# Kernel tuning notes

Hardware: AMD Instinct MI355X
Metric: run time of the kernel (lower is better)

Reference implementation:

```python
import jax, jax.numpy as jnp
import numpy as np

N = 100000      # nodes
E = 1600000     # edges (before self-loops)
D_IN = 128      # node_attr_size
H = 4           # gat_heads
C = 32          # hidden_size (per-head out channels)
F = H * C       # feature_size = 128
K = 16          # num_clusters
L = 2           # num_gat_layers
EPS = 1e-5
NEG_SLOPE = 0.2  # PyG GATv2Conv default leaky_relu slope


def setup_inputs() -> dict:
    key = jax.random.key(0)
    ks = jax.random.split(key, 8)
    x = jax.random.normal(ks[0], (N, D_IN), jnp.float32)
    edge_index = jax.random.randint(ks[1], (2, E), 0, N, jnp.int32)
    sF = 1.0 / np.sqrt(F).astype(np.float32)
    Wp = jax.random.normal(ks[2], (D_IN, F), jnp.float32) * (1.0 / np.sqrt(D_IN).astype(np.float32))
    bp = jnp.zeros((F,), jnp.float32)
    ln_g = jnp.ones((L, F), jnp.float32)
    ln_b = jnp.zeros((L, F), jnp.float32)
    Wl = jax.random.normal(ks[3], (L, F, H * C), jnp.float32) * sF
    bl = jnp.zeros((L, H * C), jnp.float32)
    Wr = jax.random.normal(ks[4], (L, F, H * C), jnp.float32) * sF
    br = jnp.zeros((L, H * C), jnp.float32)
    att = jax.random.normal(ks[5], (L, H, C), jnp.float32) * (1.0 / np.sqrt(C).astype(np.float32))
    gb = jnp.zeros((L, F), jnp.float32)  # GATv2Conv output bias
    Wc = jax.random.normal(ks[6], (F, K), jnp.float32) * sF
    bc = jnp.zeros((K,), jnp.float32)
    return dict(x=x, edge_index=edge_index, Wp=Wp, bp=bp, ln_g=ln_g, ln_b=ln_b,
                Wl=Wl, bl=bl, Wr=Wr, br=br, att=att, gb=gb, Wc=Wc, bc=bc)


def _layernorm(x, g, b):
    mu = jnp.mean(x, axis=-1, keepdims=True)
    var = jnp.var(x, axis=-1, keepdims=True)
    return (x - mu) * jax.lax.rsqrt(var + EPS) * g + b


def reference(x, edge_index, Wp, bp, ln_g, ln_b, Wl, bl, Wr, br, att, gb, Wc, bc):
    # GATv2Conv adds self-loops by default
    loops = jnp.arange(N, dtype=edge_index.dtype)
    src = jnp.concatenate([edge_index[0], loops])  # message source j
    dst = jnp.concatenate([edge_index[1], loops])  # message target i

    h = x @ Wp + bp  # node_feat_proj -> [N, F]
    for i in range(L):
        identity = h
        hn = _layernorm(h, ln_g[i], ln_b[i])
        x_l = (hn @ Wl[i] + bl[i]).reshape(N, H, C)  # source transform
        x_r = (hn @ Wr[i] + br[i]).reshape(N, H, C)  # target transform
        m = x_l[src] + x_r[dst]                       # [E+N, H, C]
        s = jnp.where(m > 0, m, NEG_SLOPE * m)        # leaky_relu(0.2)
        logits = jnp.einsum('ehc,hc->eh', s, att[i])  # [E+N, H]
        # segment softmax over incoming edges of each target node
        mx = jax.ops.segment_max(logits, dst, num_segments=N)
        a = jnp.exp(logits - mx[dst])
        den = jax.ops.segment_sum(a, dst, num_segments=N)
        alpha = a / den[dst]
        out = jax.ops.segment_sum(x_l[src] * alpha[:, :, None], dst, num_segments=N)
        out = out.reshape(N, F) + gb[i]
        # relu activation, dropout identity (eval), residual add
        h = jax.nn.relu(out) + identity

    classification_output = h @ Wc + bc
    return (classification_output, h)
```

## Files before the change

kernel.cpp:

```cpp
#include <hip/hip_runtime.h>
#include <hip/hip_bf16.h>
#include <math.h>
#include <stdint.h>

#define N_NODES 100000
#define N_EDGES 1600000
#define ET (N_EDGES + N_NODES)
#define FDIM 128
#define NK 16
#define EPS 1e-5f
#define SLOPE 0.2f

typedef __attribute__((ext_vector_type(8))) short bf16x8;
typedef __attribute__((ext_vector_type(4))) float f32x4;
typedef __attribute__((ext_vector_type(2))) _Float16 h2;

__device__ inline unsigned pk_bf16(float a, float b) {
    float2 f; f.x = a; f.y = b;
    __hip_bfloat162 t = __float22bfloat162_rn(f);
    return *reinterpret_cast<unsigned*>(&t);
}
__device__ inline h2 as_h2(unsigned u) { return __builtin_bit_cast(h2, u); }
__device__ inline unsigned as_u(h2 v) { return __builtin_bit_cast(unsigned, v); }

#define DPPF(X, CTRL) __int_as_float(__builtin_amdgcn_mov_dpp(__float_as_int(X), (CTRL), 0xF, 0xF, true))
#define DX1(X) DPPF(X, 0xB1)
#define DX2(X) DPPF(X, 0x4E)
#define DR4(X) DPPF(X, 0x124)
#define DR8(X) DPPF(X, 0x128)
#define DB0(X) DPPF(X, 0x00)
#define DB1(X) DPPF(X, 0x55)
#define DB2(X) DPPF(X, 0xAA)
#define DB3(X) DPPF(X, 0xFF)

__device__ inline float exp2_hw(float x) {
    float r;
    asm("v_exp_f32 %0, %1" : "=v"(r) : "v"(x));
    return r;
}

#define FMAMIX_LO(ACC, U, W) \
    asm("v_fma_mix_f32 %0, %1, %2, %0 op_sel_hi:[1,0,0]" : "+v"(ACC) : "v"(U), "v"(W))
#define FMAMIX_HI(ACC, U, W) \
    asm("v_fma_mix_f32 %0, %1, %2, %0 op_sel:[1,0,0] op_sel_hi:[1,0,0]" : "+v"(ACC) : "v"(U), "v"(W))

__device__ inline int rflm(int v) { return __builtin_amdgcn_readfirstlane(v) & 131071; }


#define NBKT 196
#define BSH 9
#define BSTRIDE 10240
#define P1_EPT 8
#define P1_EPB (256 * P1_EPT)

__global__ __launch_bounds__(256) void part_kernel(const int* __restrict__ ei,
                                                   int* __restrict__ gcount,
                                                   int* __restrict__ staging) {
    __shared__ int hist[NBKT];
    __shared__ int lofs[NBKT];
    __shared__ int gbase[NBKT];
    __shared__ int s[256];
    __shared__ int spk[P1_EPB];
    __shared__ short sbk[P1_EPB];
    int t = threadIdx.x;
    if (t < NBKT) hist[t] = 0;
    __syncthreads();
    int e0 = blockIdx.x * P1_EPB + t;
    int pk[P1_EPT], bk[P1_EPT], rk[P1_EPT];
#pragma unroll
    for (int k = 0; k < P1_EPT; k++) {
        int e = e0 + k * 256;
        bk[k] = -1;
        if (e < ET) {
            int src, dst;
            if (e < N_EDGES) { src = ei[e]; dst = ei[N_EDGES + e]; }
            else             { src = dst = e - N_EDGES; }
            int b = dst >> BSH;
            pk[k] = (src << BSH) | (dst & 511);
            bk[k] = b;
            rk[k] = atomicAdd(&hist[b], 1);
        }
    }
    __syncthreads();
    int v = (t < NBKT) ? hist[t] : 0;
    s[t] = v;
    __syncthreads();
    for (int o = 1; o < 256; o <<= 1) {
        int add = (t >= o) ? s[t - o] : 0;
        __syncthreads();
        s[t] += add;
        __syncthreads();
    }
    if (t < NBKT) {
        lofs[t] = s[t] - v;
        gbase[t] = (v > 0) ? atomicAdd(&gcount[t], v) : 0;
    }
    __syncthreads();
#pragma unroll
    for (int k = 0; k < P1_EPT; k++) {
        if (bk[k] >= 0) {
            int idx = lofs[bk[k]] + rk[k];
            spk[idx] = pk[k];
            sbk[idx] = (short)bk[k];
        }
    }
    __syncthreads();
    int tot = lofs[NBKT - 1] + hist[NBKT - 1];
    for (int i = t; i < tot; i += 256) {
        int b = sbk[i];
        staging[b * BSTRIDE + gbase[b] + (i - lofs[b])] = spk[i];
    }
}

__global__ __launch_bounds__(1024) void bucket_csr_kernel(
        const int* __restrict__ staging, const int* __restrict__ gcount,
        int* __restrict__ off, int* __restrict__ perm) {
    __shared__ int hist[512];
    __shared__ int scn[512];
    __shared__ int cur[512];
    __shared__ int gpre[256];
    int b = blockIdx.x;
    int t = threadIdx.x;
    if (t < 512) hist[t] = 0;
    if (t < 256) gpre[t] = (t < NBKT) ? gcount[t] : 0;
    __syncthreads();
    int sz = gcount[b];
    for (int k = t; k < sz; k += 1024)
        atomicAdd(&hist[staging[b * BSTRIDE + k] & 511], 1);
    __syncthreads();
    int v = (t < 512) ? hist[t] : 0;
    if (t < 512) scn[t] = v;
    __syncthreads();
    for (int o = 1; o < 512; o <<= 1) {
        int add = 0, gadd = 0;
        int tg = t - 512;
        if (t < 512 && t >= o) add = scn[t - o];
        if (tg >= o && tg < 256 && o < 256) gadd = gpre[tg - o];
        __syncthreads();
        if (t < 512) scn[t] += add;
        if (tg >= o && tg < 256 && o < 256) gpre[tg] += gadd;
        __syncthreads();
    }
    int base = gpre[b] - sz;
    if (t < 512) {
        int excl = scn[t] - v;
        int n = (b << BSH) + t;
        if (n < N_NODES) off[n] = base + excl;
        cur[t] = excl;
    }
    if (b == 0 && t == 0) off[N_NODES] = ET;
    __syncthreads();
    for (int k = t; k < sz; k += 1024) {
        int p = staging[b * BSTRIDE + k];
        int slot = atomicAdd(&cur[p & 511], 1);
        perm[base + slot] = p >> BSH;
    }
}


__global__ void swizzle_kernel(const float* __restrict__ Wp,
                               const float* __restrict__ Wl,
                               const float* __restrict__ Wr,
                               ushort* __restrict__ wbp,
                               ushort* __restrict__ wbl0,
                               ushort* __restrict__ wbl1) {
    int bb = blockIdx.x, t = threadIdx.x;
    const float *W0, *W1; ushort* out; int nt;
    if (bb < 8)       { W0 = Wp; W1 = Wp; out = wbp; nt = bb; }
    else if (bb < 24) { W0 = Wl; W1 = Wr; out = wbl0; nt = bb - 8; }
    else              { W0 = Wl + FDIM * FDIM; W1 = Wr + FDIM * FDIM; out = wbl1; nt = bb - 24; }
    int kk = t >> 6, lane = t & 63;
    int n = nt * 16 + (lane & 15);
    int k0 = kk * 32 + (lane >> 4) * 8;
    const float* W = (n < 128) ? (W0 + n) : (W1 + (n - 128));
    float f[8];
#pragma unroll
    for (int j = 0; j < 8; j++) f[j] = W[(size_t)(k0 + j) * FDIM];
    uint4 u;
    u.x = pk_bf16(f[0], f[1]); u.y = pk_bf16(f[2], f[3]);
    u.z = pk_bf16(f[4], f[5]); u.w = pk_bf16(f[6], f[7]);
    *(uint4*)&out[(size_t)((nt * 4 + kk) * 64 + lane) * 8] = u;
}


__global__ __launch_bounds__(256) void ln_gemm2_kernel(
        const float* __restrict__ h,
        const float* __restrict__ g, const float* __restrict__ b,
        const ushort* __restrict__ wb, const float* __restrict__ bl,
        const float* __restrict__ br,
        ushort* __restrict__ xlh, ushort* __restrict__ xrh) {
    __shared__ uint4 fragbuf[4 * 272];
    int wid = (blockIdx.x * 256 + threadIdx.x) >> 6;
    int lane = threadIdx.x & 63;
    if (wid >= N_NODES / 16) return;
    uint4* fb = fragbuf + (threadIdx.x >> 6) * 272;
    int q = lane >> 4, m = lane & 15;
    int row0 = wid * 16;
    const float* hrow = h + (size_t)(row0 + m) * FDIM + q * 32;
    float v[32];
#pragma unroll
    for (int i = 0; i < 8; i++) {
        float4 t4 = *(const float4*)&hrow[i * 4];
        v[i * 4 + 0] = t4.x; v[i * 4 + 1] = t4.y; v[i * 4 + 2] = t4.z; v[i * 4 + 3] = t4.w;
    }
    float s = 0.f, ss = 0.f;
#pragma unroll
    for (int i = 0; i < 32; i++) { s += v[i]; ss += v[i] * v[i]; }
    s  += __shfl_xor(s, 16);  s  += __shfl_xor(s, 32);
    ss += __shfl_xor(ss, 16); ss += __shfl_xor(ss, 32);
    float mu = s * (1.f / 128.f);
    float var = ss * (1.f / 128.f) - mu * mu;
    float rv = rsqrtf(var + EPS);
#pragma unroll
    for (int i = 0; i < 8; i++) {
        float4 gv = *(const float4*)&g[q * 32 + i * 4];
        float4 bv = *(const float4*)&b[q * 32 + i * 4];
        v[i * 4 + 0] = (v[i * 4 + 0] - mu) * rv * gv.x + bv.x;
        v[i * 4 + 1] = (v[i * 4 + 1] - mu) * rv * gv.y + bv.y;
        v[i * 4 + 2] = (v[i * 4 + 2] - mu) * rv * gv.z + bv.z;
        v[i * 4 + 3] = (v[i * 4 + 3] - mu) * rv * gv.w + bv.w;
    }
#pragma unroll
    for (int p = 0; p < 4; p++) {
        uint4 u;
        u.x = pk_bf16(v[p * 8 + 0], v[p * 8 + 1]);
        u.y = pk_bf16(v[p * 8 + 2], v[p * 8 + 3]);
        u.z = pk_bf16(v[p * 8 + 4], v[p * 8 + 5]);
        u.w = pk_bf16(v[p * 8 + 6], v[p * 8 + 7]);
        fb[q * 68 + p * 17 + m] = u;
    }
    bf16x8 A[4];
#pragma unroll
    for (int kk = 0; kk < 4; kk++)
        A[kk] = *(const bf16x8*)&fb[kk * 68 + q * 17 + m];
    const bf16x8* wbv = (const bf16x8*)wb;
    f32x4 acc[16];
    f32x4 z = {0.f, 0.f, 0.f, 0.f};
#pragma unroll
    for (int nt = 0; nt < 16; nt++) acc[nt] = z;
#pragma unroll
    for (int nt = 0; nt < 16; nt++) {
#pragma unroll
        for (int kk = 0; kk < 4; kk++) {
            bf16x8 B = wbv[(nt * 4 + kk) * 64 + lane];
            acc[nt] = __builtin_amdgcn_mfma_f32_16x16x32_bf16(A[kk], B, acc[nt], 0, 0, 0);
        }
    }
#pragma unroll
    for (int nt = 0; nt < 16; nt++) {
        int col = nt * 16 + m;
        if (nt < 8) {
            float bias = bl[col];
#pragma unroll
            for (int r = 0; r < 4; r++) {
                _Float16 hf = (_Float16)(acc[nt][r] + bias);
                xlh[(size_t)(row0 + q * 4 + r) * FDIM + col] = __builtin_bit_cast(ushort, hf);
            }
        } else {
            int c2 = col - 128;
            float bias = br[c2];
#pragma unroll
            for (int r = 0; r < 4; r++) {
                _Float16 hf = (_Float16)(acc[nt][r] + bias);
                xrh[(size_t)(row0 + q * 4 + r) * FDIM + c2] = __builtin_bit_cast(ushort, hf);
            }
        }
    }
}

__global__ __launch_bounds__(256) void proj_kernel(
        const float* __restrict__ x, const ushort* __restrict__ wb,
        const float* __restrict__ bp, float* __restrict__ h) {
    __shared__ uint4 fragbuf[4 * 272];
    int wid = (blockIdx.x * 256 + threadIdx.x) >> 6;
    int lane = threadIdx.x & 63;
    if (wid >= N_NODES / 16) return;
    uint4* fb = fragbuf + (threadIdx.x >> 6) * 272;
    int q = lane >> 4, m = lane & 15;
    int row0 = wid * 16;
    const float* xrow = x + (size_t)(row0 + m) * FDIM + q * 32;
#pragma unroll
    for (int p = 0; p < 4; p++) {
        float4 a = *(const float4*)&xrow[p * 8];
        float4 c = *(const float4*)&xrow[p * 8 + 4];
        uint4 u;
        u.x = pk_bf16(a.x, a.y); u.y = pk_bf16(a.z, a.w);
        u.z = pk_bf16(c.x, c.y); u.w = pk_bf16(c.z, c.w);
        fb[q * 68 + p * 17 + m] = u;
    }
    bf16x8 A[4];
#pragma unroll
    for (int kk = 0; kk < 4; kk++)
        A[kk] = *(const bf16x8*)&fb[kk * 68 + q * 17 + m];
    const bf16x8* wbv = (const bf16x8*)wb;
    f32x4 acc[8];
    f32x4 z = {0.f, 0.f, 0.f, 0.f};
#pragma unroll
    for (int nt = 0; nt < 8; nt++) acc[nt] = z;
#pragma unroll
    for (int nt = 0; nt < 8; nt++) {
#pragma unroll
        for (int kk = 0; kk < 4; kk++) {
            bf16x8 B = wbv[(nt * 4 + kk) * 64 + lane];
            acc[nt] = __builtin_amdgcn_mfma_f32_16x16x32_bf16(A[kk], B, acc[nt], 0, 0, 0);
        }
    }
#pragma unroll
    for (int nt = 0; nt < 8; nt++) {
        int col = nt * 16 + m;
        float bias = bp[col];
#pragma unroll
        for (int r = 0; r < 4; r++)
            h[(size_t)(row0 + q * 4 + r) * FDIM + col] = acc[nt][r] + bias;
    }
}

__global__ __launch_bounds__(256) void final_kernel(const float* __restrict__ h,
                                                    const float* __restrict__ Wc,
                                                    const float* __restrict__ bc,
                                                    float* __restrict__ out) {
    __shared__ float sh[16][128];
    int row0 = blockIdx.x * 16;
    int t = threadIdx.x;
    for (int i = t; i < 512; i += 256) {
        int r = i >> 5, c4 = (i & 31) * 4;
        *(float4*)&sh[r][c4] = *(const float4*)&h[(size_t)(row0 + r) * FDIM + c4];
    }
    __syncthreads();
    int m = t >> 4, k = t & 15;
    float acc = 0.f;
    for (int c = 0; c < 128; c += 4) {
        const float4 xv = *(const float4*)&sh[m][c];
        acc += xv.x * Wc[(c + 0) * NK + k] + xv.y * Wc[(c + 1) * NK + k]
             + xv.z * Wc[(c + 2) * NK + k] + xv.w * Wc[(c + 3) * NK + k];
    }
    out[(size_t)(row0 + m) * NK + k] = acc + bc[k];
}


__global__ __launch_bounds__(256) void gat_agg_kernel(
        const unsigned* __restrict__ xlp, const unsigned* __restrict__ xrp,
        const int* __restrict__ off, const int* __restrict__ perm,
        const float* __restrict__ att, const float* __restrict__ gb,
        float* __restrict__ h) {
    int wave = (blockIdx.x * 256 + threadIdx.x) >> 6;
    unsigned lane = threadIdx.x & 63;
    int iA = wave * 2;
    if (iA >= N_NODES) return;
    int iB = iA + 1;
    int2 oA = *(const int2*)&off[iA];
    int eB2 = off[iB + 1];
    h2 xrvA = as_h2(xrp[(unsigned)iA * 64u + lane]);
    h2 xrvB = as_h2(xrp[(unsigned)iB * 64u + lane]);
    const float2 hidA = *(const float2*)&h[(size_t)iA * FDIM + lane * 2];
    const float2 hidB = *(const float2*)&h[(size_t)iB * FDIM + lane * 2];
    const float2 gbv = *(const float2*)&gb[lane * 2];
    float2 attf = *(const float2*)&att[lane * 2];
    h2 attp; attp[0] = (_Float16)(attf.x * 1.44269504f);
    attp[1] = (_Float16)(attf.y * 1.44269504f);
    const h2 c06 = {(_Float16)0.6f, (_Float16)0.6f};
    const h2 c04 = {(_Float16)0.4f, (_Float16)0.4f};
    bool b0 = lane & 1, b1 = lane & 2;
    int begA = __builtin_amdgcn_readfirstlane(oA.x);
    int endA = __builtin_amdgcn_readfirstlane(oA.y);
    int begB = endA;
    int endB = __builtin_amdgcn_readfirstlane(eB2);
    const char* xlB_ = (const char*)xlp;
    unsigned laneB = lane << 2;

#define GLD(J) (*(const unsigned*)(xlB_ + ((unsigned)(J) * 256u + laneB)))

#define EDGE_PARTIAL(XRV, U, T)                                     \
    {                                                               \
        h2 mm = as_h2(U) + XRV;                                     \
        h2 am = as_h2(as_u(mm) & 0x7FFF7FFFu);                      \
        h2 sv = am * c04 + mm * c06;                                \
        T = __builtin_amdgcn_fdot2(sv, attp, 0.f, false);           \
    }

#define COMPUTE4(S, U0, U1, U2, U3)                                 \
    {                                                               \
        float t0, t1, t2, t3;                                       \
        EDGE_PARTIAL(xrv##S, U0, t0);                               \
        EDGE_PARTIAL(xrv##S, U1, t1);                               \
        EDGE_PARTIAL(xrv##S, U2, t2);                               \
        EDGE_PARTIAL(xrv##S, U3, t3);                               \
        float u   = b0 ? t1 : t0;                                   \
        float uu2 = b0 ? t0 : t1;                                   \
        u += DX1(uu2);                                              \
        float vv  = b0 ? t3 : t2;                                   \
        float vv2 = b0 ? t2 : t3;                                   \
        vv += DX1(vv2);                                             \
        float ww  = b1 ? vv : u;                                    \
        float ww2 = b1 ? u : vv;                                    \
        ww += DX2(ww2);                                             \
        ww += DR4(ww);                                              \
        ww += DR8(ww);                                              \
        float ew = exp2_hw(ww);                                     \
        dloc##S += ew;                                              \
        float w0 = DB0(ew);                                         \
        float w1 = DB1(ew);                                         \
        float w2 = DB2(ew);                                         \
        float w3 = DB3(ew);                                         \
        FMAMIX_LO(accx##S, U0, w0); FMAMIX_HI(accy##S, U0, w0);     \
        FMAMIX_LO(accx##S, U1, w1); FMAMIX_HI(accy##S, U1, w1);     \
        FMAMIX_LO(accx##S, U2, w2); FMAMIX_HI(accy##S, U2, w2);     \
        FMAMIX_LO(accx##S, U3, w3); FMAMIX_HI(accy##S, U3, w3);     \
    }

#define TAIL1(S, U)                                                 \
    {                                                               \
        float tt;                                                   \
        EDGE_PARTIAL(xrv##S, U, tt);                                \
        tt += DX1(tt);                                              \
        tt += DX2(tt);                                              \
        tt += DR4(tt);                                              \
        tt += DR8(tt);                                              \
        float w = exp2_hw(tt);                                      \
        if ((lane & 3) == 0) dloc##S += w;                          \
        FMAMIX_LO(accx##S, U, w); FMAMIX_HI(accy##S, U, w);         \
    }

    int nbA = (endA - begA) >> 2, tlA = (endA - begA) & 3;
    int nbB = (endB - begB) >> 2, tlB = (endB - begB) & 3;
    float accxA = 0.f, accyA = 0.f, dlocA = 0.f;
    float accxB = 0.f, accyB = 0.f, dlocB = 0.f;
    unsigned c0A, c1A, c2A, c3A, d0A, d1A, d2A, d3A; int4 p2A;
    unsigned c0B, c1B, c2B, c3B, d0B, d1B, d2B, d3B; int4 p2B;
    unsigned t0A = 0, t1A = 0, t2A = 0, t0B = 0, t1B = 0, t2B = 0;
    int4 p0A, p1A, ptA, p0B, p1B, ptB;

    if (nbA > 0) {
        __builtin_memcpy(&p0A, perm + begA, 16);
        __builtin_memcpy(&p1A, perm + begA + 4, 16);
        __builtin_memcpy(&p2A, perm + begA + 8, 16);
    }
    if (tlA > 0) __builtin_memcpy(&ptA, perm + begA + 4 * nbA, 16);
    if (nbB > 0) {
        __builtin_memcpy(&p0B, perm + begB, 16);
        __builtin_memcpy(&p1B, perm + begB + 4, 16);
        __builtin_memcpy(&p2B, perm + begB + 8, 16);
    }
    if (tlB > 0) __builtin_memcpy(&ptB, perm + begB + 4 * nbB, 16);
    if (nbA > 0) {
        c0A = GLD(rflm(p0A.x)); c1A = GLD(rflm(p0A.y)); c2A = GLD(rflm(p0A.z)); c3A = GLD(rflm(p0A.w));
        d0A = GLD(rflm(p1A.x)); d1A = GLD(rflm(p1A.y)); d2A = GLD(rflm(p1A.z)); d3A = GLD(rflm(p1A.w));
    }
    if (nbB > 0) {
        c0B = GLD(rflm(p0B.x)); c1B = GLD(rflm(p0B.y)); c2B = GLD(rflm(p0B.z)); c3B = GLD(rflm(p0B.w));
        d0B = GLD(rflm(p1B.x)); d1B = GLD(rflm(p1B.y)); d2B = GLD(rflm(p1B.z)); d3B = GLD(rflm(p1B.w));
    }
    if (tlA > 0) {
        t0A = GLD(rflm(ptA.x));
        if (tlA > 1) t1A = GLD(rflm(ptA.y));
        if (tlA > 2) t2A = GLD(rflm(ptA.z));
    }
    if (tlB > 0) {
        t0B = GLD(rflm(ptB.x));
        if (tlB > 1) t1B = GLD(rflm(ptB.y));
        if (tlB > 2) t2B = GLD(rflm(ptB.z));
    }

    int blkA = 0, blkB = 0;
    while (blkA + 2 < nbA && blkB + 2 < nbB) {
        unsigned e0 = GLD(rflm(p2A.x)), e1 = GLD(rflm(p2A.y));
        unsigned e2 = GLD(rflm(p2A.z)), e3 = GLD(rflm(p2A.w));
        unsigned f0 = GLD(rflm(p2B.x)), f1 = GLD(rflm(p2B.y));
        unsigned f2 = GLD(rflm(p2B.z)), f3 = GLD(rflm(p2B.w));
        __builtin_memcpy(&p2A, perm + begA + 4 * blkA + 12, 16);
        __builtin_memcpy(&p2B, perm + begB + 4 * blkB + 12, 16);
        COMPUTE4(A, c0A, c1A, c2A, c3A);
        c0A = d0A; c1A = d1A; c2A = d2A; c3A = d3A;
        d0A = e0; d1A = e1; d2A = e2; d3A = e3;
        COMPUTE4(B, c0B, c1B, c2B, c3B);
        c0B = d0B; c1B = d1B; c2B = d2B; c3B = d3B;
        d0B = f0; d1B = f1; d2B = f2; d3B = f3;
        ++blkA; ++blkB;
    }
    for (; blkA + 2 < nbA; ++blkA) {
        unsigned e0 = GLD(rflm(p2A.x)), e1 = GLD(rflm(p2A.y));
        unsigned e2 = GLD(rflm(p2A.z)), e3 = GLD(rflm(p2A.w));
        __builtin_memcpy(&p2A, perm + begA + 4 * blkA + 12, 16);
        COMPUTE4(A, c0A, c1A, c2A, c3A);
        c0A = d0A; c1A = d1A; c2A = d2A; c3A = d3A;
        d0A = e0; d1A = e1; d2A = e2; d3A = e3;
    }
    for (; blkB + 2 < nbB; ++blkB) {
        unsigned f0 = GLD(rflm(p2B.x)), f1 = GLD(rflm(p2B.y));
        unsigned f2 = GLD(rflm(p2B.z)), f3 = GLD(rflm(p2B.w));
        __builtin_memcpy(&p2B, perm + begB + 4 * blkB + 12, 16);
        COMPUTE4(B, c0B, c1B, c2B, c3B);
        c0B = d0B; c1B = d1B; c2B = d2B; c3B = d3B;
        d0B = f0; d1B = f1; d2B = f2; d3B = f3;
    }
    if (nbA >= 2) {
        COMPUTE4(A, c0A, c1A, c2A, c3A);
        c0A = d0A; c1A = d1A; c2A = d2A; c3A = d3A;
    }
    if (nbB >= 2) {
        COMPUTE4(B, c0B, c1B, c2B, c3B);
        c0B = d0B; c1B = d1B; c2B = d2B; c3B = d3B;
    }
    if (nbA >= 1) COMPUTE4(A, c0A, c1A, c2A, c3A);
    if (nbB >= 1) COMPUTE4(B, c0B, c1B, c2B, c3B);
    if (tlA > 0) {
        TAIL1(A, t0A);
        if (tlA > 1) TAIL1(A, t1A);
        if (tlA > 2) TAIL1(A, t2A);
    }
    if (tlB > 0) {
        TAIL1(B, t0B);
        if (tlB > 1) TAIL1(B, t1B);
        if (tlB > 2) TAIL1(B, t2B);
    }
#undef EDGE_PARTIAL
#undef COMPUTE4
#undef TAIL1
#undef GLD

    float denA = dlocA + DX1(dlocA);
    denA += DX2(denA);
    float invA = 1.f / denA;
    float2 resA;
    resA.x = fmaxf(accxA * invA + gbv.x, 0.f) + hidA.x;
    resA.y = fmaxf(accyA * invA + gbv.y, 0.f) + hidA.y;
    *(float2*)&h[(size_t)iA * FDIM + lane * 2] = resA;
    float denB = dlocB + DX1(dlocB);
    denB += DX2(denB);
    float invB = 1.f / denB;
    float2 resB;
    resB.x = fmaxf(accxB * invB + gbv.x, 0.f) + hidB.x;
    resB.y = fmaxf(accyB * invB + gbv.y, 0.f) + hidB.y;
    *(float2*)&h[(size_t)iB * FDIM + lane * 2] = resB;
}


extern "C" void kernel_launch(void* const* d_in, const int* in_sizes, int n_in,
                              void* d_out, int out_size, void* d_ws, size_t ws_size,
                              hipStream_t stream) {
    const float* x    = (const float*)d_in[0];
    const int*   ei   = (const int*)  d_in[1];
    const float* Wp   = (const float*)d_in[2];
    const float* bp   = (const float*)d_in[3];
    const float* ln_g = (const float*)d_in[4];
    const float* ln_b = (const float*)d_in[5];
    const float* Wl   = (const float*)d_in[6];
    const float* bl   = (const float*)d_in[7];
    const float* Wr   = (const float*)d_in[8];
    const float* br   = (const float*)d_in[9];
    const float* att  = (const float*)d_in[10];
    const float* gb   = (const float*)d_in[11];
    const float* Wc   = (const float*)d_in[12];
    const float* bc   = (const float*)d_in[13];

    float* out_cls = (float*)d_out;
    float* h = out_cls + (size_t)N_NODES * NK;

    char* w = (char*)d_ws;
    int* off    = (int*)w; w += (size_t)(N_NODES + 1) * sizeof(int);
    int* gcount = (int*)w; w += 256 * sizeof(int);
    int* perm   = (int*)w; w += (size_t)ET * sizeof(int);
    uintptr_t a = ((uintptr_t)w + 255) & ~(uintptr_t)255;
    ushort* xlh = (ushort*)a;
    ushort* xrh = xlh + (size_t)N_NODES * FDIM;
    ushort* wbp = xrh + (size_t)N_NODES * FDIM;
    ushort* wbl0 = wbp + 8 * 4 * 64 * 8;
    ushort* wbl1 = wbl0 + 16 * 4 * 64 * 8;
    int* staging = (int*)xlh;

    swizzle_kernel<<<40, 256, 0, stream>>>(Wp, Wl, Wr, wbp, wbl0, wbl1);

    hipMemsetAsync(gcount, 0, NBKT * sizeof(int), stream);
    part_kernel<<<(ET + P1_EPB - 1) / P1_EPB, 256, 0, stream>>>(ei, gcount, staging);
    bucket_csr_kernel<<<NBKT, 1024, 0, stream>>>(staging, gcount, off, perm);

    const int gw = (N_NODES / 16 + 3) / 4;
    proj_kernel<<<gw, 256, 0, stream>>>(x, wbp, bp, h);

    for (int l = 0; l < 2; ++l) {
        ln_gemm2_kernel<<<gw, 256, 0, stream>>>(
            h, ln_g + l * FDIM, ln_b + l * FDIM,
            (l == 0) ? wbl0 : wbl1, bl + l * FDIM, br + l * FDIM,
            xlh, xrh);
        gat_agg_kernel<<<(N_NODES / 2) / 4, 256, 0, stream>>>(
            (const unsigned*)xlh, (const unsigned*)xrh, off, perm,
            att + l * FDIM, gb + l * FDIM, h);
    }

    final_kernel<<<N_NODES / 16, 256, 0, stream>>>(h, Wc, bc, out_cls);
}
```

Before: 451.8 us.

## Merge setup kernels: fuse weight swizzle into partition, projection into CSR build

Folds the weight-swizzle kernel into the edge-partition kernel as extra blocks, and runs the input projection GEMM as extra blocks of the bucket CSR kernel, which drops from 1024 to 256 threads and scans two histogram entries per thread. This cuts two kernel launches and lets independent work overlap within one grid. In exchange the CSR blocks have fewer threads for their histogram and scatter loops, and the block types compete for shared memory and occupancy.

```diff
diff --git a/kernel.cpp b/kernel.cpp
--- a/kernel.cpp
+++ b/kernel.cpp
@@ -52,20 +52,44 @@
 #define BSTRIDE 10240
 #define P1_EPT 8
 #define P1_EPB (256 * P1_EPT)
-
-__global__ __launch_bounds__(256) void part_kernel(const int* __restrict__ ei,
-                                                   int* __restrict__ gcount,
-                                                   int* __restrict__ staging) {
+#define PART_BLOCKS ((ET + P1_EPB - 1) / P1_EPB)
+
+__global__ __launch_bounds__(256) void prep_kernel(
+        const int* __restrict__ ei, int* __restrict__ gcount,
+        int* __restrict__ staging,
+        const float* __restrict__ Wp, const float* __restrict__ Wl,
+        const float* __restrict__ Wr, ushort* __restrict__ wbp,
+        ushort* __restrict__ wbl0, ushort* __restrict__ wbl1) {
     __shared__ int hist[NBKT];
     __shared__ int lofs[NBKT];
     __shared__ int gbase[NBKT];
     __shared__ int s[256];
     __shared__ int spk[P1_EPB];
     __shared__ short sbk[P1_EPB];
+    int bid = blockIdx.x;
     int t = threadIdx.x;
+    if (bid >= PART_BLOCKS) {
+        int bb = bid - PART_BLOCKS;
+        const float *W0, *W1; ushort* out; int nt;
+        if (bb < 8)       { W0 = Wp; W1 = Wp; out = wbp; nt = bb; }
+        else if (bb < 24) { W0 = Wl; W1 = Wr; out = wbl0; nt = bb - 8; }
+        else              { W0 = Wl + FDIM * FDIM; W1 = Wr + FDIM * FDIM; out = wbl1; nt = bb - 24; }
+        int kk = t >> 6, lane = t & 63;
+        int n = nt * 16 + (lane & 15);
+        int k0 = kk * 32 + (lane >> 4) * 8;
+        const float* W = (n < 128) ? (W0 + n) : (W1 + (n - 128));
+        float f[8];
+#pragma unroll
+        for (int j = 0; j < 8; j++) f[j] = W[(size_t)(k0 + j) * FDIM];
+        uint4 u;
+        u.x = pk_bf16(f[0], f[1]); u.y = pk_bf16(f[2], f[3]);
+        u.z = pk_bf16(f[4], f[5]); u.w = pk_bf16(f[6], f[7]);
+        *(uint4*)&out[(size_t)((nt * 4 + kk) * 64 + lane) * 8] = u;
+        return;
+    }
     if (t < NBKT) hist[t] = 0;
     __syncthreads();
-    int e0 = blockIdx.x * P1_EPB + t;
+    int e0 = bid * P1_EPB + t;
     int pk[P1_EPT], bk[P1_EPT], rk[P1_EPT];
 #pragma unroll
     for (int k = 0; k < P1_EPT; k++) {
@@ -112,74 +136,95 @@
     }
 }
 
-__global__ __launch_bounds__(1024) void bucket_csr_kernel(
+__global__ __launch_bounds__(256) void csr_proj_kernel(
         const int* __restrict__ staging, const int* __restrict__ gcount,
-        int* __restrict__ off, int* __restrict__ perm) {
-    __shared__ int hist[512];
-    __shared__ int scn[512];
-    __shared__ int cur[512];
-    __shared__ int gpre[256];
-    int b = blockIdx.x;
+        int* __restrict__ off, int* __restrict__ perm,
+        const float* __restrict__ x, const ushort* __restrict__ wb,
+        const float* __restrict__ bp, float* __restrict__ h) {
+    __shared__ uint4 fragbuf[4 * 272];
+    int bid = blockIdx.x;
     int t = threadIdx.x;
-    if (t < 512) hist[t] = 0;
-    if (t < 256) gpre[t] = (t < NBKT) ? gcount[t] : 0;
+    if (bid >= NBKT) {
+        int wid = ((bid - NBKT) * 256 + t) >> 6;
+        int lane = t & 63;
+        if (wid >= N_NODES / 16) return;
+        uint4* fb = fragbuf + (t >> 6) * 272;
+        int q = lane >> 4, m = lane & 15;
+        int row0 = wid * 16;
+        const float* xrow = x + (size_t)(row0 + m) * FDIM + q * 32;
+#pragma unroll
+        for (int p = 0; p < 4; p++) {
+            float4 a = *(const float4*)&xrow[p * 8];
+            float4 c = *(const float4*)&xrow[p * 8 + 4];
+            uint4 u;
+            u.x = pk_bf16(a.x, a.y); u.y = pk_bf16(a.z, a.w);
+            u.z = pk_bf16(c.x, c.y); u.w = pk_bf16(c.z, c.w);
+            fb[q * 68 + p * 17 + m] = u;
+        }
+        bf16x8 A[4];
+#pragma unroll
+        for (int kk = 0; kk < 4; kk++)
+            A[kk] = *(const bf16x8*)&fb[kk * 68 + q * 17 + m];
+        const bf16x8* wbv = (const bf16x8*)wb;
+        f32x4 acc[8];
+        f32x4 z = {0.f, 0.f, 0.f, 0.f};
+#pragma unroll
+        for (int nt = 0; nt < 8; nt++) acc[nt] = z;
+#pragma unroll
+        for (int nt = 0; nt < 8; nt++) {
+#pragma unroll
+            for (int kk = 0; kk < 4; kk++) {
+                bf16x8 B = wbv[(nt * 4 + kk) * 64 + lane];
+                acc[nt] = __builtin_amdgcn_mfma_f32_16x16x32_bf16(A[kk], B, acc[nt], 0, 0, 0);
+            }
+        }
+#pragma unroll
+        for (int nt = 0; nt < 8; nt++) {
+            int col = nt * 16 + m;
+            float bias = bp[col];
+#pragma unroll
+            for (int r = 0; r < 4; r++)
+                h[(size_t)(row0 + q * 4 + r) * FDIM + col] = acc[nt][r] + bias;
+        }
+        return;
+    }
+    int* hist = (int*)fragbuf;
+    int* cur  = hist + 512;
+    int* pr   = cur + 512;
+    int* gpre = pr + 256;
+    int b = bid;
+    hist[t] = 0; hist[t + 256] = 0;
+    gpre[t] = (t < NBKT) ? gcount[t] : 0;
     __syncthreads();
     int sz = gcount[b];
-    for (int k = t; k < sz; k += 1024)
+    for (int k = t; k < sz; k += 256)
         atomicAdd(&hist[staging[b * BSTRIDE + k] & 511], 1);
     __syncthreads();
-    int v = (t < 512) ? hist[t] : 0;
-    if (t < 512) scn[t] = v;
-    __syncthreads();
-    for (int o = 1; o < 512; o <<= 1) {
-        int add = 0, gadd = 0;
-        int tg = t - 512;
-        if (t < 512 && t >= o) add = scn[t - o];
-        if (tg >= o && tg < 256 && o < 256) gadd = gpre[tg - o];
+    int a0 = hist[2 * t], a1 = hist[2 * t + 1];
+    pr[t] = a0 + a1;
+    __syncthreads();
+    for (int o = 1; o < 256; o <<= 1) {
+        int ad = (t >= o) ? pr[t - o] : 0;
+        int gd = (t >= o) ? gpre[t - o] : 0;
         __syncthreads();
-        if (t < 512) scn[t] += add;
-        if (tg >= o && tg < 256 && o < 256) gpre[tg] += gadd;
+        pr[t] += ad;
+        gpre[t] += gd;
         __syncthreads();
     }
     int base = gpre[b] - sz;
-    if (t < 512) {
-        int excl = scn[t] - v;
-        int n = (b << BSH) + t;
-        if (n < N_NODES) off[n] = base + excl;
-        cur[t] = excl;
-    }
+    int pe = pr[t] - (a0 + a1);
+    cur[2 * t] = pe;
+    cur[2 * t + 1] = pe + a0;
+    int n = (b << BSH) + 2 * t;
+    if (n < N_NODES)     off[n]     = base + pe;
+    if (n + 1 < N_NODES) off[n + 1] = base + pe + a0;
     if (b == 0 && t == 0) off[N_NODES] = ET;
     __syncthreads();
-    for (int k = t; k < sz; k += 1024) {
+    for (int k = t; k < sz; k += 256) {
         int p = staging[b * BSTRIDE + k];
         int slot = atomicAdd(&cur[p & 511], 1);
         perm[base + slot] = p >> BSH;
     }
-}
-
-
-__global__ void swizzle_kernel(const float* __restrict__ Wp,
-                               const float* __restrict__ Wl,
-                               const float* __restrict__ Wr,
-                               ushort* __restrict__ wbp,
-                               ushort* __restrict__ wbl0,
-                               ushort* __restrict__ wbl1) {
-    int bb = blockIdx.x, t = threadIdx.x;
-    const float *W0, *W1; ushort* out; int nt;
-    if (bb < 8)       { W0 = Wp; W1 = Wp; out = wbp; nt = bb; }
-    else if (bb < 24) { W0 = Wl; W1 = Wr; out = wbl0; nt = bb - 8; }
-    else              { W0 = Wl + FDIM * FDIM; W1 = Wr + FDIM * FDIM; out = wbl1; nt = bb - 24; }
-    int kk = t >> 6, lane = t & 63;
-    int n = nt * 16 + (lane & 15);
-    int k0 = kk * 32 + (lane >> 4) * 8;
-    const float* W = (n < 128) ? (W0 + n) : (W1 + (n - 128));
-    float f[8];
-#pragma unroll
-    for (int j = 0; j < 8; j++) f[j] = W[(size_t)(k0 + j) * FDIM];
-    uint4 u;
-    u.x = pk_bf16(f[0], f[1]); u.y = pk_bf16(f[2], f[3]);
-    u.z = pk_bf16(f[4], f[5]); u.w = pk_bf16(f[6], f[7]);
-    *(uint4*)&out[(size_t)((nt * 4 + kk) * 64 + lane) * 8] = u;
 }
 
 
@@ -265,53 +310,6 @@
                 xrh[(size_t)(row0 + q * 4 + r) * FDIM + c2] = __builtin_bit_cast(ushort, hf);
             }
         }
-    }
-}
-
-__global__ __launch_bounds__(256) void proj_kernel(
-        const float* __restrict__ x, const ushort* __restrict__ wb,
-        const float* __restrict__ bp, float* __restrict__ h) {
-    __shared__ uint4 fragbuf[4 * 272];
-    int wid = (blockIdx.x * 256 + threadIdx.x) >> 6;
-    int lane = threadIdx.x & 63;
-    if (wid >= N_NODES / 16) return;
-    uint4* fb = fragbuf + (threadIdx.x >> 6) * 272;
-    int q = lane >> 4, m = lane & 15;
-    int row0 = wid * 16;
-    const float* xrow = x + (size_t)(row0 + m) * FDIM + q * 32;
-#pragma unroll
-    for (int p = 0; p < 4; p++) {
-        float4 a = *(const float4*)&xrow[p * 8];
-        float4 c = *(const float4*)&xrow[p * 8 + 4];
-        uint4 u;
-        u.x = pk_bf16(a.x, a.y); u.y = pk_bf16(a.z, a.w);
-        u.z = pk_bf16(c.x, c.y); u.w = pk_bf16(c.z, c.w);
-        fb[q * 68 + p * 17 + m] = u;
-    }
-    bf16x8 A[4];
-#pragma unroll
-    for (int kk = 0; kk < 4; kk++)
-        A[kk] = *(const bf16x8*)&fb[kk * 68 + q * 17 + m];
-    const bf16x8* wbv = (const bf16x8*)wb;
-    f32x4 acc[8];
-    f32x4 z = {0.f, 0.f, 0.f, 0.f};
-#pragma unroll
-    for (int nt = 0; nt < 8; nt++) acc[nt] = z;
-#pragma unroll
-    for (int nt = 0; nt < 8; nt++) {
-#pragma unroll
-        for (int kk = 0; kk < 4; kk++) {
-            bf16x8 B = wbv[(nt * 4 + kk) * 64 + lane];
-            acc[nt] = __builtin_amdgcn_mfma_f32_16x16x32_bf16(A[kk], B, acc[nt], 0, 0, 0);
-        }
-    }
-#pragma unroll
-    for (int nt = 0; nt < 8; nt++) {
-        int col = nt * 16 + m;
-        float bias = bp[col];
-#pragma unroll
-        for (int r = 0; r < 4; r++)
-            h[(size_t)(row0 + q * 4 + r) * FDIM + col] = acc[nt][r] + bias;
     }
 }
 
@@ -568,15 +566,13 @@
     ushort* wbl1 = wbl0 + 16 * 4 * 64 * 8;
     int* staging = (int*)xlh;
 
-    swizzle_kernel<<<40, 256, 0, stream>>>(Wp, Wl, Wr, wbp, wbl0, wbl1);
-
     hipMemsetAsync(gcount, 0, NBKT * sizeof(int), stream);
-    part_kernel<<<(ET + P1_EPB - 1) / P1_EPB, 256, 0, stream>>>(ei, gcount, staging);
-    bucket_csr_kernel<<<NBKT, 1024, 0, stream>>>(staging, gcount, off, perm);
+    prep_kernel<<<PART_BLOCKS + 40, 256, 0, stream>>>(
+        ei, gcount, staging, Wp, Wl, Wr, wbp, wbl0, wbl1);
+    csr_proj_kernel<<<NBKT + (N_NODES / 16 + 3) / 4, 256, 0, stream>>>(
+        staging, gcount, off, perm, x, wbp, bp, h);
 
     const int gw = (N_NODES / 16 + 3) / 4;
-    proj_kernel<<<gw, 256, 0, stream>>>(x, wbp, bp, h);
-
     for (int l = 0; l < 2; ++l) {
         ln_gemm2_kernel<<<gw, 256, 0, stream>>>(
             h, ln_g + l * FDIM, ln_b + l * FDIM,
```

New measurement: 445.0 us. About the same (-1.5%).
